# Optimization experiments

Measured on AMD Instinct MI355X. Metric: run time of the kernel, lower is better.

## Reference

```python
import jax, jax.numpy as jnp
import numpy as np
import math

D_MODEL = 1024
HEADS = 16
D_K = D_MODEL // HEADS
NUM_TURNS = 30
VOCAB_B = NUM_TURNS ** 2  # 900


def setup_inputs() -> dict:
    key = jax.random.key(0)
    ks = jax.random.split(key, 16)
    bs, Lq, Lk = 4, 512, 2048
    q = jax.random.normal(ks[0], (bs, Lq, D_MODEL), jnp.float32)
    k = jax.random.normal(ks[1], (bs, Lk, D_MODEL), jnp.float32)
    v = jax.random.normal(ks[2], (bs, Lk, D_MODEL), jnp.float32)
    b_idx = jax.random.randint(ks[3], (bs, Lq, Lk), 0, VOCAB_B, jnp.int32)
    mask = jax.random.randint(ks[4], (bs, Lq, Lk), 0, 2, jnp.int32)
    s = 1.0 / math.sqrt(D_MODEL)
    Wq = jax.random.normal(ks[5], (D_MODEL, D_MODEL), jnp.float32) * s
    bq = jnp.zeros((D_MODEL,), jnp.float32)
    Wk = jax.random.normal(ks[6], (D_MODEL, D_MODEL), jnp.float32) * s
    bk = jnp.zeros((D_MODEL,), jnp.float32)
    Wv = jax.random.normal(ks[7], (D_MODEL, D_MODEL), jnp.float32) * s
    bv = jnp.zeros((D_MODEL,), jnp.float32)
    Wo = jax.random.normal(ks[8], (D_MODEL, D_MODEL), jnp.float32) * s
    bo = jnp.zeros((D_MODEL,), jnp.float32)
    # bias embedding table, padding_idx=0 -> zero row
    b_table = jax.random.normal(ks[9], (VOCAB_B, HEADS), jnp.float32) * 0.02
    b_table = b_table.at[0].set(0.0)
    return {"q": q, "k": k, "v": v, "b_idx": b_idx, "mask": mask,
            "Wq": Wq, "bq": bq, "Wk": Wk, "bk": bk, "Wv": Wv, "bv": bv,
            "Wo": Wo, "bo": bo, "b_table": b_table}


def reference(q, k, v, b_idx, mask, Wq, bq, Wk, bk, Wv, bv, Wo, bo, b_table):
    bs, Lq, _ = q.shape
    Lk = k.shape[1]
    # projections, reshape to (bs, h, L, d_k)
    qh = (q @ Wq.T + bq).reshape(bs, Lq, HEADS, D_K).transpose(0, 2, 1, 3)
    kh = (k @ Wk.T + bk).reshape(bs, Lk, HEADS, D_K).transpose(0, 2, 1, 3)
    vh = (v @ Wv.T + bv).reshape(bs, Lk, HEADS, D_K).transpose(0, 2, 1, 3)
    # learned additive bias: embedding lookup (bs,Lq,Lk,h) -> (bs,h,Lq,Lk)
    b = b_table[b_idx].transpose(0, 3, 1, 2)
    scores = jnp.einsum('bhqd,bhkd->bhqk', qh, kh) / math.sqrt(D_K) + b
    scores = jnp.where(mask[:, None] == 0, jnp.float32(-1e9), scores)
    attn = jax.nn.softmax(scores, axis=-1)
    out = jnp.einsum('bhqk,bhkd->bhqd', attn, vh)
    out = out.transpose(0, 2, 1, 3).reshape(bs, Lq, D_MODEL)
    return out @ Wo.T + bo
```

## Files before the change

kernel.cpp:

```cpp
#include <hip/hip_runtime.h>
#include <hip/hip_bf16.h>

#define H 16
#define DK 64
#define DM 1024
#define LQ 512
#define LK 2048
#define BSZ 4

typedef __hip_bfloat16 bf16;
typedef __attribute__((ext_vector_type(8))) short short8;
typedef __attribute__((ext_vector_type(4))) short short4v;
typedef __attribute__((ext_vector_type(4))) float f32x4;

#define LOG2E 1.44269504f
#define SC2 0.18033688f


__global__ __launch_bounds__(256) void fused_cvt(
    const float* __restrict__ q, const float* __restrict__ k, const float* __restrict__ v,
    const int* __restrict__ bidx, const int* __restrict__ msk,
    const float* __restrict__ Wq, const float* __restrict__ Wk,
    const float* __restrict__ Wv, const float* __restrict__ Wo,
    const float* __restrict__ btab,
    bf16* __restrict__ qb, bf16* __restrict__ kb, bf16* __restrict__ vb,
    bf16* __restrict__ Wqb, bf16* __restrict__ Wkb, bf16* __restrict__ Wvb,
    bf16* __restrict__ Wob, short* __restrict__ pkd, float* __restrict__ btabT) {
  const int blk = blockIdx.x, tid = threadIdx.x;
  const float* src;
  bf16* dst;
  int base;
  if (blk < 2048)       { src = q;  dst = qb;  base = blk; }
  else if (blk < 10240) { src = k;  dst = kb;  base = blk - 2048; }
  else if (blk < 18432) { src = v;  dst = vb;  base = blk - 10240; }
  else if (blk < 19456) { src = Wq; dst = Wqb; base = blk - 18432; }
  else if (blk < 20480) { src = Wk; dst = Wkb; base = blk - 19456; }
  else if (blk < 21504) { src = Wv; dst = Wvb; base = blk - 20480; }
  else if (blk < 22528) { src = Wo; dst = Wob; base = blk - 21504; }
  else if (blk < 26624) {
    int i = (blk - 22528) * 1024 + tid * 4;
    int4 a = *reinterpret_cast<const int4*>(bidx + i);
    int4 m = *reinterpret_cast<const int4*>(msk + i);
    short4 r;
    r.x = m.x ? (short)a.x : (short)900;
    r.y = m.y ? (short)a.y : (short)900;
    r.z = m.z ? (short)a.z : (short)900;
    r.w = m.w ? (short)a.w : (short)900;
    *reinterpret_cast<short4*>(pkd + i) = r;
    return;
  } else {
    for (int j = tid; j < H * 901; j += 256) {
      int hh = j / 901, i = j - hh * 901;
      btabT[j] = (i == 900) ? -1e9f : (btab[i * H + hh] - 10.0f) * LOG2E;
    }
    return;
  }
  int i = base * 1024 + tid * 4;
  float4 val = *reinterpret_cast<const float4*>(src + i);
  bf16 o0 = __float2bfloat16(val.x), o1 = __float2bfloat16(val.y);
  bf16 o2 = __float2bfloat16(val.z), o3 = __float2bfloat16(val.w);
  short4 pk;
  pk.x = *reinterpret_cast<short*>(&o0);
  pk.y = *reinterpret_cast<short*>(&o1);
  pk.z = *reinterpret_cast<short*>(&o2);
  pk.w = *reinterpret_cast<short*>(&o3);
  *reinterpret_cast<short4*>(reinterpret_cast<short*>(dst) + i) = pk;
}


__device__ __forceinline__ void g2lds16(const bf16* g, bf16* l) {
  __builtin_amdgcn_global_load_lds(
      (__attribute__((address_space(1))) void*)(g),
      (__attribute__((address_space(3))) void*)(l), 16, 0, 0);
}

template <int MODE, int TM>
__device__ __forceinline__ void gemm_body(bf16* __restrict__ As, bf16* __restrict__ Bs,
                                          const bf16* __restrict__ A,
                                          const bf16* __restrict__ B,
                                          const float* __restrict__ bias,
                                          void* __restrict__ out,
                                          int M, int N, int K, int Lrows,
                                          int bx, int by) {
  constexpr int NT = (TM == 128) ? 4 : 2;
  const int tid = threadIdx.x;
  const int wave = tid >> 6, lane = tid & 63;
  const int quad = lane >> 4, l15 = lane & 15;
  const int rowbase = (TM == 128) ? (wave >> 1) * 64 : 0;
  const int colbase = (TM == 128) ? (wave & 1) * 64 : wave * 32;
  const int rowA0 = bx * TM, colB0 = by * 128;
  const int srow = lane >> 2, skq = lane & 3;

  f32x4 acc[4][NT];
  const f32x4 zero = {0.f, 0.f, 0.f, 0.f};
  for (int mt = 0; mt < 4; mt++)
    for (int nt = 0; nt < NT; nt++) acc[mt][nt] = zero;

  for (int k0 = 0; k0 < K; k0 += 32) {
    if (TM == 128) {
      for (int c = 0; c < 2; ++c) {
        int r = wave * 32 + c * 16;
        g2lds16(A + (size_t)(rowA0 + r + srow) * K + k0 + skq * 8, As + r * 32);
      }
    } else {
      int r = wave * 16;
      g2lds16(A + (size_t)(rowA0 + r + srow) * K + k0 + skq * 8, As + r * 32);
    }
    for (int c = 0; c < 2; ++c) {
      int r = wave * 32 + c * 16;
      g2lds16(B + (size_t)(colB0 + r + srow) * K + k0 + skq * 8, Bs + r * 32);
    }
    __syncthreads();
    short8 af[4], bfr[NT];
    for (int mt = 0; mt < 4; mt++)
      af[mt] = *reinterpret_cast<const short8*>(As + (rowbase + mt * 16 + l15) * 32 + quad * 8);
    for (int nt = 0; nt < NT; nt++)
      bfr[nt] = *reinterpret_cast<const short8*>(Bs + (colbase + nt * 16 + l15) * 32 + quad * 8);
    for (int mt = 0; mt < 4; mt++)
      for (int nt = 0; nt < NT; nt++) {
        if (MODE == 1)
          acc[mt][nt] = __builtin_amdgcn_mfma_f32_16x16x32_bf16(bfr[nt], af[mt], acc[mt][nt], 0, 0, 0);
        else
          acc[mt][nt] = __builtin_amdgcn_mfma_f32_16x16x32_bf16(af[mt], bfr[nt], acc[mt][nt], 0, 0, 0);
      }
    __syncthreads();
  }

  const int bb = (MODE == 2) ? 0 : (rowA0 / Lrows);
  const int lb = (MODE == 2) ? rowA0 : (rowA0 - bb * Lrows);
  if (MODE == 1) {
    for (int mt = 0; mt < 4; mt++) {
      int key = lb + rowbase + mt * 16 + l15;
      for (int nt = 0; nt < NT; nt++) {
        f32x4 v = acc[mt][nt];
        for (int r = 0; r < 4; r++) {
          int ncol = colB0 + colbase + nt * 16 + quad * 4 + r;
          float bv = bias[ncol];
          int hh = ncol >> 6, d = ncol & 63;
          ((bf16*)out)[((size_t)((bb * H + hh) * DK + d)) * LK + key] =
              __float2bfloat16(v[r] + bv);
        }
      }
    }
    return;
  }
  for (int nt = 0; nt < NT; nt++) {
    int col = colB0 + colbase + nt * 16 + l15;
    float bv = bias[col];
    int hh = col >> 6, d = col & 63;
    for (int mt = 0; mt < 4; mt++) {
      int lrow0 = lb + rowbase + mt * 16 + quad * 4;
      f32x4 v = acc[mt][nt];
      for (int r = 0; r < 4; r++) {
        float val = v[r] + bv;
        if (MODE == 0) {
          ((bf16*)out)[(((size_t)(bb * H + hh) * Lrows + lrow0 + r) << 6) + d] = __float2bfloat16(val);
        } else {
          ((float*)out)[(size_t)(lrow0 + r) * N + col] = val;
        }
      }
    }
  }
}

__global__ __launch_bounds__(256) void proj_qkv(
    const bf16* __restrict__ kb, const bf16* __restrict__ Wkb, const float* __restrict__ bk, bf16* __restrict__ Kh,
    const bf16* __restrict__ vb, const bf16* __restrict__ Wvb, const float* __restrict__ bv, bf16* __restrict__ Vt,
    const bf16* __restrict__ qb, const bf16* __restrict__ Wqb, const float* __restrict__ bq, bf16* __restrict__ Qh) {
  __shared__ __align__(16) bf16 As[128 * 32];
  __shared__ __align__(16) bf16 Bs[128 * 32];
  const int blk = blockIdx.x;
  if (blk < 512) {
    const int xcd = blk & 7, slot = blk >> 3;
    gemm_body<0, 128>(As, Bs, kb, Wkb, bk, (void*)Kh, 8192, 1024, 1024, LK,
                      xcd * 8 + (slot & 7), slot >> 3);
  } else if (blk < 1024) {
    const int i = blk - 512, xcd = i & 7, slot = i >> 3;
    gemm_body<1, 128>(As, Bs, vb, Wvb, bv, (void*)Vt, 8192, 1024, 1024, LK,
                      xcd * 8 + (slot & 7), slot >> 3);
  } else {
    const int i = blk - 1024, xcd = i & 7, slot = i >> 3;
    gemm_body<0, 64>(As, Bs, qb, Wqb, bq, (void*)Qh, 2048, 1024, 1024, LQ,
                     xcd * 4 + (slot & 3), slot >> 2);
  }
}

__global__ __launch_bounds__(256) void gemm_o(const bf16* __restrict__ A,
                                              const bf16* __restrict__ B,
                                              const float* __restrict__ bias,
                                              float* __restrict__ out) {
  __shared__ __align__(16) bf16 As[64 * 32];
  __shared__ __align__(16) bf16 Bs[128 * 32];
  const int blk = blockIdx.x, xcd = blk & 7, slot = blk >> 3;
  gemm_body<2, 64>(As, Bs, A, B, bias, (void*)out, 2048, 1024, 1024, LQ,
                   xcd * 4 + (slot & 3), slot >> 2);
}


__global__ __launch_bounds__(512) void attn9(const bf16* __restrict__ Qh,
                                             const bf16* __restrict__ Kh,
                                             const bf16* __restrict__ Vt,
                                             const short* __restrict__ pkm,
                                             const float* __restrict__ btabT,
                                             float* __restrict__ Opart,
                                             float* __restrict__ L) {
  __shared__ __align__(16) bf16 Kbuf[2][64 * 64];
  __shared__ __align__(16) bf16 Vbuf[2][64 * 64];
  __shared__ float bts[901];
  const int tid = threadIdx.x;
  const int wave = tid >> 6, lane = tid & 63;
  const int quad = lane >> 4, l15 = lane & 15;
  const int bh = blockIdx.x, b = bh >> 4, h = bh & 15;
  const int qt = blockIdx.y, z = blockIdx.z;
  const int key_base = z * 1024;

  for (int i = tid; i < 901; i += 512) bts[i] = btabT[h * 901 + i];

  const int q = qt * 128 + wave * 16 + l15;
  short8 qf[2];
  for (int ks = 0; ks < 2; ks++)
    qf[ks] = *reinterpret_cast<const short8*>(
        Qh + ((size_t)bh * LQ + q) * DK + ks * 32 + quad * 8);

  const bf16* kbase = Kh + ((size_t)bh * LK + key_base) * DK;
  const bf16* vbase = Vt + ((size_t)bh * DK) * LK + key_base;
  const short* pkrow = pkm + ((size_t)b * LQ + q) * LK + key_base;

  const int srow_off = lane >> 3;
  const int sseg = ((lane & 7) - srow_off) & 7;
  const int srow = wave * 8 + srow_off;

  f32x4 of[4];
  float denom = 0.f;
  const f32x4 zero = {0.f, 0.f, 0.f, 0.f};
  for (int dt = 0; dt < 4; dt++) of[dt] = zero;

  g2lds16(kbase + (size_t)srow * DK + sseg * 8, &Kbuf[0][(wave * 8) * 64]);
  g2lds16(vbase + (size_t)srow * LK + sseg * 8, &Vbuf[0][(wave * 8) * 64]);
  short4v pkv[4];
  for (int nt = 0; nt < 4; nt++)
    pkv[nt] = *reinterpret_cast<const short4v*>(pkrow + nt * 16 + quad * 4);

  __syncthreads();

  for (int kc = 0; kc < 16; ++kc) {
    const int buf = kc & 1;

    short4v pk_n[4];
    if (kc < 15) {
      const int key1 = (kc + 1) * 64;
      g2lds16(kbase + (size_t)(key1 + srow) * DK + sseg * 8,
              &Kbuf[buf ^ 1][(wave * 8) * 64]);
      g2lds16(vbase + (size_t)srow * LK + key1 + sseg * 8,
              &Vbuf[buf ^ 1][(wave * 8) * 64]);
      for (int nt = 0; nt < 4; nt++)
        pk_n[nt] = *reinterpret_cast<const short4v*>(pkrow + key1 + nt * 16 + quad * 4);
    }

    f32x4 sa[4];
    for (int nt = 0; nt < 4; nt++) sa[nt] = zero;
    for (int nt = 0; nt < 4; nt++)
      for (int ks = 0; ks < 2; ks++) {
        short8 kf = *reinterpret_cast<const short8*>(
            &Kbuf[buf][(nt * 16 + l15) * 64 + (((ks * 4 + quad + l15) & 7) << 3)]);
        sa[nt] = __builtin_amdgcn_mfma_f32_16x16x32_bf16(kf, qf[ks], sa[nt], 0, 0, 0);
      }

    short4v vf[4][4];
    for (int dt = 0; dt < 4; dt++)
      for (int nt = 0; nt < 4; nt++)
        vf[dt][nt] = *reinterpret_cast<const short4v*>(
            &Vbuf[buf][(dt * 16 + l15) * 64 +
                       (((nt * 2 + (quad >> 1) + l15) & 7) << 3) + ((quad & 1) << 2)]);

    short4v pf[4];
    for (int nt = 0; nt < 4; nt++) {
      float p[4];
      for (int r = 0; r < 4; r++) {
        float t = fmaf(sa[nt][r], SC2, bts[pkv[nt][r]]);
        p[r] = __builtin_amdgcn_exp2f(t);
      }
      denom += (p[0] + p[1]) + (p[2] + p[3]);
      short4v pk4;
      for (int r = 0; r < 4; r++) {
        bf16 tb = __float2bfloat16(p[r]);
        pk4[r] = *reinterpret_cast<short*>(&tb);
      }
      pf[nt] = pk4;
    }

    for (int dt = 0; dt < 4; dt++)
      for (int nt = 0; nt < 4; nt++)
        of[dt] = __builtin_amdgcn_mfma_f32_16x16x16bf16_1k(vf[dt][nt], pf[nt], of[dt], 0, 0, 0);

    if (kc < 15)
      for (int nt = 0; nt < 4; nt++) pkv[nt] = pk_n[nt];

    __syncthreads();
  }

  denom += __shfl_xor(denom, 16, 64);
  denom += __shfl_xor(denom, 32, 64);

  size_t rowi = ((size_t)z * 64 + bh) * LQ + q;
  float* orow = Opart + rowi * 64;
  for (int dt = 0; dt < 4; dt++)
    *reinterpret_cast<f32x4*>(orow + dt * 16 + quad * 4) = of[dt];
  if (quad == 0) L[rowi] = denom;
}

__global__ __launch_bounds__(256) void attn_combine(const float* __restrict__ Opart,
                                                    const float* __restrict__ L,
                                                    bf16* __restrict__ Ob) {
  int t = blockIdx.x * 256 + threadIdx.x;
  int g = t * 4;
  int row = g >> 6, d0 = g & 63;
  float l = L[row] + L[32768 + row];
  float4 o;
  float4 p0 = *reinterpret_cast<const float4*>(Opart + ((size_t)row << 6) + d0);
  float4 p1 = *reinterpret_cast<const float4*>(Opart + (((size_t)32768 + row) << 6) + d0);
  o.x = p0.x + p1.x; o.y = p0.y + p1.y; o.z = p0.z + p1.z; o.w = p0.w + p1.w;
  float inv = 1.f / l;
  bf16 t0 = __float2bfloat16(o.x * inv), t1 = __float2bfloat16(o.y * inv);
  bf16 t2 = __float2bfloat16(o.z * inv), t3 = __float2bfloat16(o.w * inv);
  short4 pk;
  pk.x = *reinterpret_cast<short*>(&t0);
  pk.y = *reinterpret_cast<short*>(&t1);
  pk.z = *reinterpret_cast<short*>(&t2);
  pk.w = *reinterpret_cast<short*>(&t3);
  int bh = row >> 9, qq = row & 511, b_ = bh >> 4, h = bh & 15;
  *reinterpret_cast<short4*>(Ob + ((size_t)(b_ * LQ + qq)) * DM + h * 64 + d0) = pk;
}


extern "C" void kernel_launch(void* const* d_in, const int* in_sizes, int n_in,
                              void* d_out, int out_size, void* d_ws, size_t ws_size,
                              hipStream_t stream) {
  const float* q = (const float*)d_in[0];
  const float* k = (const float*)d_in[1];
  const float* v = (const float*)d_in[2];
  const int* bidx = (const int*)d_in[3];
  const int* mask = (const int*)d_in[4];
  const float* Wq = (const float*)d_in[5];
  const float* bq = (const float*)d_in[6];
  const float* Wk = (const float*)d_in[7];
  const float* bk = (const float*)d_in[8];
  const float* Wv = (const float*)d_in[9];
  const float* bv = (const float*)d_in[10];
  const float* Wo = (const float*)d_in[11];
  const float* bo = (const float*)d_in[12];
  const float* btab = (const float*)d_in[13];

  char* ws = (char*)d_ws;
  bf16* qb  = (bf16*)(ws + 0);
  bf16* kb  = (bf16*)(ws + 4194304);
  bf16* vb  = (bf16*)(ws + 20971520);
  bf16* Wqb = (bf16*)(ws + 37748736);
  bf16* Wkb = (bf16*)(ws + 39845888);
  bf16* Wvb = (bf16*)(ws + 41943040);
  bf16* Wob = (bf16*)(ws + 44040192);
  bf16* Qh  = (bf16*)(ws + 46137344);
  bf16* Kh  = (bf16*)(ws + 50331648);
  bf16* Vt  = (bf16*)(ws + 67108864);
  short* pkd = (short*)(ws + 83886080);
  bf16* Ob  = (bf16*)(ws + 92274688);
  float* btabT = (float*)(ws + 92274688);
  float* Opart = (float*)(ws + 0);
  float* L     = (float*)(ws + 16777216);
  (void)ws_size; (void)in_sizes; (void)n_in; (void)out_size;

  hipLaunchKernelGGL(fused_cvt, dim3(26625), dim3(256), 0, stream,
                     q, k, v, bidx, mask, Wq, Wk, Wv, Wo, btab,
                     qb, kb, vb, Wqb, Wkb, Wvb, Wob, pkd, btabT);

  hipLaunchKernelGGL(proj_qkv, dim3(1280), dim3(256), 0, stream,
                     kb, Wkb, bk, Kh, vb, Wvb, bv, Vt, qb, Wqb, bq, Qh);

  hipLaunchKernelGGL(attn9, dim3(BSZ * H, LQ / 128, 2), dim3(512), 0, stream,
                     Qh, Kh, Vt, pkd, btabT, Opart, L);
  hipLaunchKernelGGL(attn_combine, dim3(2048), dim3(256), 0, stream,
                     Opart, L, Ob);

  hipLaunchKernelGGL(gemm_o, dim3(256), dim3(256), 0, stream,
                     Ob, Wob, bo, (float*)d_out);
}
```

Before: 308.8 us.

## Double-buffer LDS tiles in GEMM body to overlap loads with MFMA

The shared GEMM body now stages A/B k-slices into two LDS buffers, issuing the next slice's global-to-LDS loads before computing on the current one. This is meant to hide global memory latency behind the MFMA work in the projection and output GEMMs. It doubles LDS use per block, which may lower occupancy, and the synchronization at the loop end is not visible here, so correctness depends on barriers the hidden code still has.

Result: no change. 309.0 us (+0.1%).

```diff
diff --git a/kernel.cpp b/kernel.cpp
--- a/kernel.cpp
+++ b/kernel.cpp
@@ -96,26 +96,39 @@
   for (int mt = 0; mt < 4; mt++)
     for (int nt = 0; nt < NT; nt++) acc[mt][nt] = zero;
 
-  for (int k0 = 0; k0 < K; k0 += 32) {
+  auto stage = [&](int buf, int k0) {
+    bf16* Ad = As + buf * (TM * 32);
+    bf16* Bd = Bs + buf * (128 * 32);
     if (TM == 128) {
       for (int c = 0; c < 2; ++c) {
         int r = wave * 32 + c * 16;
-        g2lds16(A + (size_t)(rowA0 + r + srow) * K + k0 + skq * 8, As + r * 32);
+        g2lds16(A + (size_t)(rowA0 + r + srow) * K + k0 + skq * 8, Ad + r * 32);
       }
     } else {
       int r = wave * 16;
-      g2lds16(A + (size_t)(rowA0 + r + srow) * K + k0 + skq * 8, As + r * 32);
+      g2lds16(A + (size_t)(rowA0 + r + srow) * K + k0 + skq * 8, Ad + r * 32);
     }
     for (int c = 0; c < 2; ++c) {
       int r = wave * 32 + c * 16;
-      g2lds16(B + (size_t)(colB0 + r + srow) * K + k0 + skq * 8, Bs + r * 32);
-    }
-    __syncthreads();
+      g2lds16(B + (size_t)(colB0 + r + srow) * K + k0 + skq * 8, Bd + r * 32);
+    }
+  };
+
+  stage(0, 0);
+  __syncthreads();
+
+  const int NKS = K / 32;
+  for (int t = 0; t < NKS; ++t) {
+    const int cur = t & 1;
+    if (t + 1 < NKS) stage(cur ^ 1, (t + 1) * 32);
+
+    const bf16* Ac = As + cur * (TM * 32);
+    const bf16* Bc = Bs + cur * (128 * 32);
     short8 af[4], bfr[NT];
     for (int mt = 0; mt < 4; mt++)
-      af[mt] = *reinterpret_cast<const short8*>(As + (rowbase + mt * 16 + l15) * 32 + quad * 8);
+      af[mt] = *reinterpret_cast<const short8*>(Ac + (rowbase + mt * 16 + l15) * 32 + quad * 8);
     for (int nt = 0; nt < NT; nt++)
-      bfr[nt] = *reinterpret_cast<const short8*>(Bs + (colbase + nt * 16 + l15) * 32 + quad * 8);
+      bfr[nt] = *reinterpret_cast<const short8*>(Bc + (colbase + nt * 16 + l15) * 32 + quad * 8);
     for (int mt = 0; mt < 4; mt++)
       for (int nt = 0; nt < NT; nt++) {
         if (MODE == 1)
@@ -167,8 +180,8 @@
     const bf16* __restrict__ kb, const bf16* __restrict__ Wkb, const float* __restrict__ bk, bf16* __restrict__ Kh,
     const bf16* __restrict__ vb, const bf16* __restrict__ Wvb, const float* __restrict__ bv, bf16* __restrict__ Vt,
     const bf16* __restrict__ qb, const bf16* __restrict__ Wqb, const float* __restrict__ bq, bf16* __restrict__ Qh) {
-  __shared__ __align__(16) bf16 As[128 * 32];
-  __shared__ __align__(16) bf16 Bs[128 * 32];
+  __shared__ __align__(16) bf16 As[2 * 128 * 32];
+  __shared__ __align__(16) bf16 Bs[2 * 128 * 32];
   const int blk = blockIdx.x;
   if (blk < 512) {
     const int xcd = blk & 7, slot = blk >> 3;
@@ -189,8 +202,8 @@
                                               const bf16* __restrict__ B,
                                               const float* __restrict__ bias,
                                               float* __restrict__ out) {
-  __shared__ __align__(16) bf16 As[64 * 32];
-  __shared__ __align__(16) bf16 Bs[128 * 32];
+  __shared__ __align__(16) bf16 As[2 * 64 * 32];
+  __shared__ __align__(16) bf16 Bs[2 * 128 * 32];
   const int blk = blockIdx.x, xcd = blk & 7, slot = blk >> 3;
   gemm_body<2, 64>(As, Bs, A, B, bias, (void*)out, 2048, 1024, 1024, LQ,
                    xcd * 4 + (slot & 3), slot >> 2);
```

## Fuse fp32-to-bf16 activation conversion into QKV projection GEMM loads

Applied to the files above, without the earlier changes.

Drops the separate pass that converted q, k and v activations to bf16. The projection GEMM now loads fp32 activation tiles straight into LDS using a rotated (swizzled) layout and converts them to bf16 while building MFMA fragments. This removes a full read and write of the bf16 activation copies (about 34M elements). In exchange, the GEMM reads twice the bytes for A, uses twice the LDS for the A tile, and does conversion work inside the inner loop.

After: 342.4 us. 1.11x slower.

```diff
diff --git a/kernel.cpp b/kernel.cpp
--- a/kernel.cpp
+++ b/kernel.cpp
@@ -18,27 +18,33 @@
 
 
 __global__ __launch_bounds__(256) void fused_cvt(
-    const float* __restrict__ q, const float* __restrict__ k, const float* __restrict__ v,
     const int* __restrict__ bidx, const int* __restrict__ msk,
     const float* __restrict__ Wq, const float* __restrict__ Wk,
     const float* __restrict__ Wv, const float* __restrict__ Wo,
     const float* __restrict__ btab,
-    bf16* __restrict__ qb, bf16* __restrict__ kb, bf16* __restrict__ vb,
     bf16* __restrict__ Wqb, bf16* __restrict__ Wkb, bf16* __restrict__ Wvb,
     bf16* __restrict__ Wob, short* __restrict__ pkd, float* __restrict__ btabT) {
   const int blk = blockIdx.x, tid = threadIdx.x;
-  const float* src;
-  bf16* dst;
-  int base;
-  if (blk < 2048)       { src = q;  dst = qb;  base = blk; }
-  else if (blk < 10240) { src = k;  dst = kb;  base = blk - 2048; }
-  else if (blk < 18432) { src = v;  dst = vb;  base = blk - 10240; }
-  else if (blk < 19456) { src = Wq; dst = Wqb; base = blk - 18432; }
-  else if (blk < 20480) { src = Wk; dst = Wkb; base = blk - 19456; }
-  else if (blk < 21504) { src = Wv; dst = Wvb; base = blk - 20480; }
-  else if (blk < 22528) { src = Wo; dst = Wob; base = blk - 21504; }
-  else if (blk < 26624) {
-    int i = (blk - 22528) * 1024 + tid * 4;
+  if (blk < 4096) {
+    const float* src;
+    bf16* dst;
+    const int w = blk >> 10, base = blk & 1023;
+    if (w == 0)      { src = Wq; dst = Wqb; }
+    else if (w == 1) { src = Wk; dst = Wkb; }
+    else if (w == 2) { src = Wv; dst = Wvb; }
+    else             { src = Wo; dst = Wob; }
+    int i = base * 1024 + tid * 4;
+    float4 val = *reinterpret_cast<const float4*>(src + i);
+    bf16 o0 = __float2bfloat16(val.x), o1 = __float2bfloat16(val.y);
+    bf16 o2 = __float2bfloat16(val.z), o3 = __float2bfloat16(val.w);
+    short4 pk;
+    pk.x = *reinterpret_cast<short*>(&o0);
+    pk.y = *reinterpret_cast<short*>(&o1);
+    pk.z = *reinterpret_cast<short*>(&o2);
+    pk.w = *reinterpret_cast<short*>(&o3);
+    *reinterpret_cast<short4*>(reinterpret_cast<short*>(dst) + i) = pk;
+  } else if (blk < 8192) {
+    int i = (blk - 4096) * 1024 + tid * 4;
     int4 a = *reinterpret_cast<const int4*>(bidx + i);
     int4 m = *reinterpret_cast<const int4*>(msk + i);
     short4 r;
@@ -47,36 +53,24 @@
     r.z = m.z ? (short)a.z : (short)900;
     r.w = m.w ? (short)a.w : (short)900;
     *reinterpret_cast<short4*>(pkd + i) = r;
-    return;
   } else {
     for (int j = tid; j < H * 901; j += 256) {
       int hh = j / 901, i = j - hh * 901;
       btabT[j] = (i == 900) ? -1e9f : (btab[i * H + hh] - 10.0f) * LOG2E;
     }
-    return;
-  }
-  int i = base * 1024 + tid * 4;
-  float4 val = *reinterpret_cast<const float4*>(src + i);
-  bf16 o0 = __float2bfloat16(val.x), o1 = __float2bfloat16(val.y);
-  bf16 o2 = __float2bfloat16(val.z), o3 = __float2bfloat16(val.w);
-  short4 pk;
-  pk.x = *reinterpret_cast<short*>(&o0);
-  pk.y = *reinterpret_cast<short*>(&o1);
-  pk.z = *reinterpret_cast<short*>(&o2);
-  pk.w = *reinterpret_cast<short*>(&o3);
-  *reinterpret_cast<short4*>(reinterpret_cast<short*>(dst) + i) = pk;
-}
-
-
-__device__ __forceinline__ void g2lds16(const bf16* g, bf16* l) {
+  }
+}
+
+
+__device__ __forceinline__ void g2lds16(const void* g, void* l) {
   __builtin_amdgcn_global_load_lds(
       (__attribute__((address_space(1))) void*)(g),
       (__attribute__((address_space(3))) void*)(l), 16, 0, 0);
 }
 
-template <int MODE, int TM>
-__device__ __forceinline__ void gemm_body(bf16* __restrict__ As, bf16* __restrict__ Bs,
-                                          const bf16* __restrict__ A,
+template <int MODE, int TM, bool AF32>
+__device__ __forceinline__ void gemm_body(void* __restrict__ AsRaw, bf16* __restrict__ Bs,
+                                          const void* __restrict__ A,
                                           const bf16* __restrict__ B,
                                           const float* __restrict__ bias,
                                           void* __restrict__ out,
@@ -97,14 +91,27 @@
     for (int nt = 0; nt < NT; nt++) acc[mt][nt] = zero;
 
   for (int k0 = 0; k0 < K; k0 += 32) {
-    if (TM == 128) {
-      for (int c = 0; c < 2; ++c) {
-        int r = wave * 32 + c * 16;
-        g2lds16(A + (size_t)(rowA0 + r + srow) * K + k0 + skq * 8, As + r * 32);
+    if (AF32) {
+      const float* A32 = (const float*)A;
+      float* Ad32 = (float*)AsRaw;
+      const int ro = lane >> 3;
+      const int gs = ((lane & 7) - ro) & 7;
+      for (int c = 0; c < TM / 32; ++c) {
+        int rbase = wave * (TM / 4) + c * 8;
+        g2lds16(A32 + (size_t)(rowA0 + rbase + ro) * K + k0 + gs * 4,
+                Ad32 + rbase * 32);
       }
     } else {
-      int r = wave * 16;
-      g2lds16(A + (size_t)(rowA0 + r + srow) * K + k0 + skq * 8, As + r * 32);
+      bf16* Ad = (bf16*)AsRaw;
+      if (TM == 128) {
+        for (int c = 0; c < 2; ++c) {
+          int r = wave * 32 + c * 16;
+          g2lds16((const bf16*)A + (size_t)(rowA0 + r + srow) * K + k0 + skq * 8, Ad + r * 32);
+        }
+      } else {
+        int r = wave * 16;
+        g2lds16((const bf16*)A + (size_t)(rowA0 + r + srow) * K + k0 + skq * 8, Ad + r * 32);
+      }
     }
     for (int c = 0; c < 2; ++c) {
       int r = wave * 32 + c * 16;
@@ -112,8 +119,25 @@
     }
     __syncthreads();
     short8 af[4], bfr[NT];
-    for (int mt = 0; mt < 4; mt++)
-      af[mt] = *reinterpret_cast<const short8*>(As + (rowbase + mt * 16 + l15) * 32 + quad * 8);
+    for (int mt = 0; mt < 4; mt++) {
+      const int r = rowbase + mt * 16 + l15;
+      if (AF32) {
+        const float* Ac32 = (const float*)AsRaw;
+        const int s0 = (quad * 2 + l15) & 7, s1 = (quad * 2 + 1 + l15) & 7;
+        f32x4 a0 = *reinterpret_cast<const f32x4*>(Ac32 + r * 32 + s0 * 4);
+        f32x4 a1 = *reinterpret_cast<const f32x4*>(Ac32 + r * 32 + s1 * 4);
+        short8 t;
+        for (int j = 0; j < 4; j++) {
+          bf16 b0 = __float2bfloat16(a0[j]);
+          bf16 b1 = __float2bfloat16(a1[j]);
+          t[j] = *reinterpret_cast<short*>(&b0);
+          t[4 + j] = *reinterpret_cast<short*>(&b1);
+        }
+        af[mt] = t;
+      } else {
+        af[mt] = *reinterpret_cast<const short8*>((const bf16*)AsRaw + r * 32 + quad * 8);
+      }
+    }
     for (int nt = 0; nt < NT; nt++)
       bfr[nt] = *reinterpret_cast<const short8*>(Bs + (colbase + nt * 16 + l15) * 32 + quad * 8);
     for (int mt = 0; mt < 4; mt++)
@@ -164,24 +188,24 @@
 }
 
 __global__ __launch_bounds__(256) void proj_qkv(
-    const bf16* __restrict__ kb, const bf16* __restrict__ Wkb, const float* __restrict__ bk, bf16* __restrict__ Kh,
-    const bf16* __restrict__ vb, const bf16* __restrict__ Wvb, const float* __restrict__ bv, bf16* __restrict__ Vt,
-    const bf16* __restrict__ qb, const bf16* __restrict__ Wqb, const float* __restrict__ bq, bf16* __restrict__ Qh) {
-  __shared__ __align__(16) bf16 As[128 * 32];
+    const float* __restrict__ k, const bf16* __restrict__ Wkb, const float* __restrict__ bk, bf16* __restrict__ Kh,
+    const float* __restrict__ v, const bf16* __restrict__ Wvb, const float* __restrict__ bv, bf16* __restrict__ Vt,
+    const float* __restrict__ q, const bf16* __restrict__ Wqb, const float* __restrict__ bq, bf16* __restrict__ Qh) {
+  __shared__ __align__(16) char AsRaw[128 * 32 * 4];
   __shared__ __align__(16) bf16 Bs[128 * 32];
   const int blk = blockIdx.x;
   if (blk < 512) {
     const int xcd = blk & 7, slot = blk >> 3;
-    gemm_body<0, 128>(As, Bs, kb, Wkb, bk, (void*)Kh, 8192, 1024, 1024, LK,
-                      xcd * 8 + (slot & 7), slot >> 3);
+    gemm_body<0, 128, true>(AsRaw, Bs, k, Wkb, bk, (void*)Kh, 8192, 1024, 1024, LK,
+                            xcd * 8 + (slot & 7), slot >> 3);
   } else if (blk < 1024) {
     const int i = blk - 512, xcd = i & 7, slot = i >> 3;
-    gemm_body<1, 128>(As, Bs, vb, Wvb, bv, (void*)Vt, 8192, 1024, 1024, LK,
-                      xcd * 8 + (slot & 7), slot >> 3);
+    gemm_body<1, 128, true>(AsRaw, Bs, v, Wvb, bv, (void*)Vt, 8192, 1024, 1024, LK,
+                            xcd * 8 + (slot & 7), slot >> 3);
   } else {
     const int i = blk - 1024, xcd = i & 7, slot = i >> 3;
-    gemm_body<0, 64>(As, Bs, qb, Wqb, bq, (void*)Qh, 2048, 1024, 1024, LQ,
-                     xcd * 4 + (slot & 3), slot >> 2);
+    gemm_body<0, 64, true>(AsRaw, Bs, q, Wqb, bq, (void*)Qh, 2048, 1024, 1024, LQ,
+                           xcd * 4 + (slot & 3), slot >> 2);
   }
 }
 
@@ -189,11 +213,11 @@
                                               const bf16* __restrict__ B,
                                               const float* __restrict__ bias,
                                               float* __restrict__ out) {
-  __shared__ __align__(16) bf16 As[64 * 32];
+  __shared__ __align__(16) char AsRaw[64 * 32 * 2];
   __shared__ __align__(16) bf16 Bs[128 * 32];
   const int blk = blockIdx.x, xcd = blk & 7, slot = blk >> 3;
-  gemm_body<2, 64>(As, Bs, A, B, bias, (void*)out, 2048, 1024, 1024, LQ,
-                   xcd * 4 + (slot & 3), slot >> 2);
+  gemm_body<2, 64, false>(AsRaw, Bs, A, B, bias, (void*)out, 2048, 1024, 1024, LQ,
+                          xcd * 4 + (slot & 3), slot >> 2);
 }
 
 
@@ -352,9 +376,6 @@
   const float* btab = (const float*)d_in[13];
 
   char* ws = (char*)d_ws;
-  bf16* qb  = (bf16*)(ws + 0);
-  bf16* kb  = (bf16*)(ws + 4194304);
-  bf16* vb  = (bf16*)(ws + 20971520);
   bf16* Wqb = (bf16*)(ws + 37748736);
   bf16* Wkb = (bf16*)(ws + 39845888);
   bf16* Wvb = (bf16*)(ws + 41943040);
@@ -369,12 +390,12 @@
   float* L     = (float*)(ws + 16777216);
   (void)ws_size; (void)in_sizes; (void)n_in; (void)out_size;
 
-  hipLaunchKernelGGL(fused_cvt, dim3(26625), dim3(256), 0, stream,
-                     q, k, v, bidx, mask, Wq, Wk, Wv, Wo, btab,
-                     qb, kb, vb, Wqb, Wkb, Wvb, Wob, pkd, btabT);
+  hipLaunchKernelGGL(fused_cvt, dim3(8193), dim3(256), 0, stream,
+                     bidx, mask, Wq, Wk, Wv, Wo, btab,
+                     Wqb, Wkb, Wvb, Wob, pkd, btabT);
 
   hipLaunchKernelGGL(proj_qkv, dim3(1280), dim3(256), 0, stream,
-                     kb, Wkb, bk, Kh, vb, Wvb, bv, Vt, qb, Wqb, bq, Qh);
+                     k, Wkb, bk, Kh, v, Wvb, bv, Vt, q, Wqb, bq, Qh);
 
   hipLaunchKernelGGL(attn9, dim3(BSZ * H, LQ / 128, 2), dim3(512), 0, stream,
                      Qh, Kh, Vt, pkd, btabT, Opart, L);
```

## Fuse split-K attention combine into output projection and widen conversion blocks

Applied to the files above, without the earlier changes.

Removes the attn_combine kernel. The output-projection GEMM now reads both fp32 partial outputs and their denominators directly, normalizes them, converts to bf16 and stores the result in LDS as its A operand. This saves one launch and the write and re-read of the bf16 intermediate. The cost is that the A tile is now loaded synchronously from fp32 data instead of with async global-to-LDS loads, and each row's partial outputs are re-read by every column block. Separately, the conversion kernel now handles four float4s per thread, so it launches far fewer blocks.

Result: slower. 318.2 us (+3.0%).

```diff
diff --git a/kernel.cpp b/kernel.cpp
--- a/kernel.cpp
+++ b/kernel.cpp
@@ -16,6 +16,17 @@
 #define LOG2E 1.44269504f
 #define SC2 0.18033688f
 
+
+__device__ __forceinline__ short4 cvt4(float4 v) {
+  bf16 o0 = __float2bfloat16(v.x), o1 = __float2bfloat16(v.y);
+  bf16 o2 = __float2bfloat16(v.z), o3 = __float2bfloat16(v.w);
+  short4 pk;
+  pk.x = *reinterpret_cast<short*>(&o0);
+  pk.y = *reinterpret_cast<short*>(&o1);
+  pk.z = *reinterpret_cast<short*>(&o2);
+  pk.w = *reinterpret_cast<short*>(&o3);
+  return pk;
+}
 
 __global__ __launch_bounds__(256) void fused_cvt(
     const float* __restrict__ q, const float* __restrict__ k, const float* __restrict__ v,
@@ -27,48 +38,52 @@
     bf16* __restrict__ Wqb, bf16* __restrict__ Wkb, bf16* __restrict__ Wvb,
     bf16* __restrict__ Wob, short* __restrict__ pkd, float* __restrict__ btabT) {
   const int blk = blockIdx.x, tid = threadIdx.x;
-  const float* src;
-  bf16* dst;
-  int base;
-  if (blk < 2048)       { src = q;  dst = qb;  base = blk; }
-  else if (blk < 10240) { src = k;  dst = kb;  base = blk - 2048; }
-  else if (blk < 18432) { src = v;  dst = vb;  base = blk - 10240; }
-  else if (blk < 19456) { src = Wq; dst = Wqb; base = blk - 18432; }
-  else if (blk < 20480) { src = Wk; dst = Wkb; base = blk - 19456; }
-  else if (blk < 21504) { src = Wv; dst = Wvb; base = blk - 20480; }
-  else if (blk < 22528) { src = Wo; dst = Wob; base = blk - 21504; }
-  else if (blk < 26624) {
-    int i = (blk - 22528) * 1024 + tid * 4;
-    int4 a = *reinterpret_cast<const int4*>(bidx + i);
-    int4 m = *reinterpret_cast<const int4*>(msk + i);
-    short4 r;
-    r.x = m.x ? (short)a.x : (short)900;
-    r.y = m.y ? (short)a.y : (short)900;
-    r.z = m.z ? (short)a.z : (short)900;
-    r.w = m.w ? (short)a.w : (short)900;
-    *reinterpret_cast<short4*>(pkd + i) = r;
-    return;
+  if (blk < 5632) {
+    const float* src;
+    bf16* dst;
+    int base;
+    if (blk < 512)       { src = q;  dst = qb;  base = blk; }
+    else if (blk < 2560) { src = k;  dst = kb;  base = blk - 512; }
+    else if (blk < 4608) { src = v;  dst = vb;  base = blk - 2560; }
+    else {
+      const int wi = blk - 4608, w = wi >> 8;
+      base = wi & 255;
+      src = (w == 0) ? Wq : (w == 1) ? Wk : (w == 2) ? Wv : Wo;
+      dst = (w == 0) ? Wqb : (w == 1) ? Wkb : (w == 2) ? Wvb : Wob;
+    }
+    const float4* s = reinterpret_cast<const float4*>(src) + (size_t)base * 1024 + tid;
+    short4* d = reinterpret_cast<short4*>(dst) + (size_t)base * 1024 + tid;
+    float4 v0 = s[0], v1 = s[256], v2 = s[512], v3 = s[768];
+    d[0] = cvt4(v0);
+    d[256] = cvt4(v1);
+    d[512] = cvt4(v2);
+    d[768] = cvt4(v3);
+  } else if (blk < 6656) {
+    const int base = blk - 5632;
+    const int4* sa = reinterpret_cast<const int4*>(bidx) + (size_t)base * 1024 + tid;
+    const int4* sm = reinterpret_cast<const int4*>(msk) + (size_t)base * 1024 + tid;
+    short4* d = reinterpret_cast<short4*>(pkd) + (size_t)base * 1024 + tid;
+#pragma unroll
+    for (int it = 0; it < 4; ++it) {
+      int4 a = sa[it * 256];
+      int4 m = sm[it * 256];
+      short4 r;
+      r.x = m.x ? (short)a.x : (short)900;
+      r.y = m.y ? (short)a.y : (short)900;
+      r.z = m.z ? (short)a.z : (short)900;
+      r.w = m.w ? (short)a.w : (short)900;
+      d[it * 256] = r;
+    }
   } else {
     for (int j = tid; j < H * 901; j += 256) {
       int hh = j / 901, i = j - hh * 901;
       btabT[j] = (i == 900) ? -1e9f : (btab[i * H + hh] - 10.0f) * LOG2E;
     }
-    return;
-  }
-  int i = base * 1024 + tid * 4;
-  float4 val = *reinterpret_cast<const float4*>(src + i);
-  bf16 o0 = __float2bfloat16(val.x), o1 = __float2bfloat16(val.y);
-  bf16 o2 = __float2bfloat16(val.z), o3 = __float2bfloat16(val.w);
-  short4 pk;
-  pk.x = *reinterpret_cast<short*>(&o0);
-  pk.y = *reinterpret_cast<short*>(&o1);
-  pk.z = *reinterpret_cast<short*>(&o2);
-  pk.w = *reinterpret_cast<short*>(&o3);
-  *reinterpret_cast<short4*>(reinterpret_cast<short*>(dst) + i) = pk;
-}
-
-
-__device__ __forceinline__ void g2lds16(const bf16* g, bf16* l) {
+  }
+}
+
+
+__device__ __forceinline__ void g2lds16(const void* g, void* l) {
   __builtin_amdgcn_global_load_lds(
       (__attribute__((address_space(1))) void*)(g),
       (__attribute__((address_space(3))) void*)(l), 16, 0, 0);
@@ -76,9 +91,10 @@
 
 template <int MODE, int TM>
 __device__ __forceinline__ void gemm_body(bf16* __restrict__ As, bf16* __restrict__ Bs,
-                                          const bf16* __restrict__ A,
+                                          const void* __restrict__ A,
                                           const bf16* __restrict__ B,
                                           const float* __restrict__ bias,
+                                          const float* __restrict__ Lp,
                                           void* __restrict__ out,
                                           int M, int N, int K, int Lrows,
                                           int bx, int by) {
@@ -97,14 +113,37 @@
     for (int nt = 0; nt < NT; nt++) acc[mt][nt] = zero;
 
   for (int k0 = 0; k0 < K; k0 += 32) {
-    if (TM == 128) {
+    if (MODE == 3) {
+      const float* Op = (const float*)A;
+      const int r = wave * 16 + srow;
+      const int row = rowA0 + r;
+      const int b_ = row >> 9, qq = row & 511;
+      const int c0 = k0 + skq * 8;
+      const int h = c0 >> 6, d0 = c0 & 63;
+      const size_t ri = (size_t)(b_ * 16 + h) * 512 + qq;
+      const float inv = 1.f / (Lp[ri] + Lp[32768 + ri]);
+      const float* p0 = Op + ri * 64 + d0;
+      const float* p1 = Op + (size_t)(32768 + ri) * 64 + d0;
+      f32x4 a0 = *reinterpret_cast<const f32x4*>(p0);
+      f32x4 a1 = *reinterpret_cast<const f32x4*>(p0 + 4);
+      f32x4 b0 = *reinterpret_cast<const f32x4*>(p1);
+      f32x4 b1 = *reinterpret_cast<const f32x4*>(p1 + 4);
+      short8 wv;
+      for (int j = 0; j < 4; j++) {
+        bf16 x = __float2bfloat16((a0[j] + b0[j]) * inv);
+        bf16 y = __float2bfloat16((a1[j] + b1[j]) * inv);
+        wv[j] = *reinterpret_cast<short*>(&x);
+        wv[4 + j] = *reinterpret_cast<short*>(&y);
+      }
+      *reinterpret_cast<short8*>(As + r * 32 + skq * 8) = wv;
+    } else if (TM == 128) {
       for (int c = 0; c < 2; ++c) {
         int r = wave * 32 + c * 16;
-        g2lds16(A + (size_t)(rowA0 + r + srow) * K + k0 + skq * 8, As + r * 32);
+        g2lds16((const bf16*)A + (size_t)(rowA0 + r + srow) * K + k0 + skq * 8, As + r * 32);
       }
     } else {
       int r = wave * 16;
-      g2lds16(A + (size_t)(rowA0 + r + srow) * K + k0 + skq * 8, As + r * 32);
+      g2lds16((const bf16*)A + (size_t)(rowA0 + r + srow) * K + k0 + skq * 8, As + r * 32);
     }
     for (int c = 0; c < 2; ++c) {
       int r = wave * 32 + c * 16;
@@ -126,8 +165,8 @@
     __syncthreads();
   }
 
-  const int bb = (MODE == 2) ? 0 : (rowA0 / Lrows);
-  const int lb = (MODE == 2) ? rowA0 : (rowA0 - bb * Lrows);
+  const int bb = (MODE >= 2) ? 0 : (rowA0 / Lrows);
+  const int lb = (MODE >= 2) ? rowA0 : (rowA0 - bb * Lrows);
   if (MODE == 1) {
     for (int mt = 0; mt < 4; mt++) {
       int key = lb + rowbase + mt * 16 + l15;
@@ -172,27 +211,28 @@
   const int blk = blockIdx.x;
   if (blk < 512) {
     const int xcd = blk & 7, slot = blk >> 3;
-    gemm_body<0, 128>(As, Bs, kb, Wkb, bk, (void*)Kh, 8192, 1024, 1024, LK,
+    gemm_body<0, 128>(As, Bs, kb, Wkb, bk, nullptr, (void*)Kh, 8192, 1024, 1024, LK,
                       xcd * 8 + (slot & 7), slot >> 3);
   } else if (blk < 1024) {
     const int i = blk - 512, xcd = i & 7, slot = i >> 3;
-    gemm_body<1, 128>(As, Bs, vb, Wvb, bv, (void*)Vt, 8192, 1024, 1024, LK,
+    gemm_body<1, 128>(As, Bs, vb, Wvb, bv, nullptr, (void*)Vt, 8192, 1024, 1024, LK,
                       xcd * 8 + (slot & 7), slot >> 3);
   } else {
     const int i = blk - 1024, xcd = i & 7, slot = i >> 3;
-    gemm_body<0, 64>(As, Bs, qb, Wqb, bq, (void*)Qh, 2048, 1024, 1024, LQ,
+    gemm_body<0, 64>(As, Bs, qb, Wqb, bq, nullptr, (void*)Qh, 2048, 1024, 1024, LQ,
                      xcd * 4 + (slot & 3), slot >> 2);
   }
 }
 
-__global__ __launch_bounds__(256) void gemm_o(const bf16* __restrict__ A,
+__global__ __launch_bounds__(256) void gemm_o(const float* __restrict__ Opart,
                                               const bf16* __restrict__ B,
                                               const float* __restrict__ bias,
+                                              const float* __restrict__ Lp,
                                               float* __restrict__ out) {
   __shared__ __align__(16) bf16 As[64 * 32];
   __shared__ __align__(16) bf16 Bs[128 * 32];
   const int blk = blockIdx.x, xcd = blk & 7, slot = blk >> 3;
-  gemm_body<2, 64>(As, Bs, A, B, bias, (void*)out, 2048, 1024, 1024, LQ,
+  gemm_body<3, 64>(As, Bs, Opart, B, bias, Lp, (void*)out, 2048, 1024, 1024, LQ,
                    xcd * 4 + (slot & 3), slot >> 2);
 }
 
@@ -307,29 +347,6 @@
   for (int dt = 0; dt < 4; dt++)
     *reinterpret_cast<f32x4*>(orow + dt * 16 + quad * 4) = of[dt];
   if (quad == 0) L[rowi] = denom;
-}
-
-__global__ __launch_bounds__(256) void attn_combine(const float* __restrict__ Opart,
-                                                    const float* __restrict__ L,
-                                                    bf16* __restrict__ Ob) {
-  int t = blockIdx.x * 256 + threadIdx.x;
-  int g = t * 4;
-  int row = g >> 6, d0 = g & 63;
-  float l = L[row] + L[32768 + row];
-  float4 o;
-  float4 p0 = *reinterpret_cast<const float4*>(Opart + ((size_t)row << 6) + d0);
-  float4 p1 = *reinterpret_cast<const float4*>(Opart + (((size_t)32768 + row) << 6) + d0);
-  o.x = p0.x + p1.x; o.y = p0.y + p1.y; o.z = p0.z + p1.z; o.w = p0.w + p1.w;
-  float inv = 1.f / l;
-  bf16 t0 = __float2bfloat16(o.x * inv), t1 = __float2bfloat16(o.y * inv);
-  bf16 t2 = __float2bfloat16(o.z * inv), t3 = __float2bfloat16(o.w * inv);
-  short4 pk;
-  pk.x = *reinterpret_cast<short*>(&t0);
-  pk.y = *reinterpret_cast<short*>(&t1);
-  pk.z = *reinterpret_cast<short*>(&t2);
-  pk.w = *reinterpret_cast<short*>(&t3);
-  int bh = row >> 9, qq = row & 511, b_ = bh >> 4, h = bh & 15;
-  *reinterpret_cast<short4*>(Ob + ((size_t)(b_ * LQ + qq)) * DM + h * 64 + d0) = pk;
 }
 
 
@@ -363,13 +380,12 @@
   bf16* Kh  = (bf16*)(ws + 50331648);
   bf16* Vt  = (bf16*)(ws + 67108864);
   short* pkd = (short*)(ws + 83886080);
-  bf16* Ob  = (bf16*)(ws + 92274688);
   float* btabT = (float*)(ws + 92274688);
   float* Opart = (float*)(ws + 0);
   float* L     = (float*)(ws + 16777216);
   (void)ws_size; (void)in_sizes; (void)n_in; (void)out_size;
 
-  hipLaunchKernelGGL(fused_cvt, dim3(26625), dim3(256), 0, stream,
+  hipLaunchKernelGGL(fused_cvt, dim3(6657), dim3(256), 0, stream,
                      q, k, v, bidx, mask, Wq, Wk, Wv, Wo, btab,
                      qb, kb, vb, Wqb, Wkb, Wvb, Wob, pkd, btabT);
 
@@ -378,9 +394,7 @@
 
   hipLaunchKernelGGL(attn9, dim3(BSZ * H, LQ / 128, 2), dim3(512), 0, stream,
                      Qh, Kh, Vt, pkd, btabT, Opart, L);
-  hipLaunchKernelGGL(attn_combine, dim3(2048), dim3(256), 0, stream,
-                     Opart, L, Ob);
 
   hipLaunchKernelGGL(gemm_o, dim3(256), dim3(256), 0, stream,
-                     Ob, Wob, bo, (float*)d_out);
-}
+                     Opart, Wob, bo, L, (float*)d_out);
+}
```
